# Kernel tuning notes

Measured on AMD Instinct MI355X. Metric: run time of the kernel, lower is better.

The kernel has to match this reference:

```python
import jax, jax.numpy as jnp
import numpy as np

B, OBS, T, H = 4096, 16, 32, 512  # batch, encoder length, decode seq_len, hidden_size


def _lstm_cell(x, h, c, Wi, Wh, b):
    # PyTorch gate order: i, f, g, o. b = b_ih + b_hh (mathematically identical).
    g = x @ Wi.T + h @ Wh.T + b
    i, f, gg, o = jnp.split(g, 4, axis=-1)
    c = jax.nn.sigmoid(f) * c + jax.nn.sigmoid(i) * jnp.tanh(gg)
    h = jax.nn.sigmoid(o) * jnp.tanh(c)
    return h, c


def _encode(xs, Wi, Wh, b):
    # xs: [B, T, 4]; returns final (h, c), zero initial state as in nn.LSTM.
    def step(carry, x):
        h, c = _lstm_cell(x, carry[0], carry[1], Wi, Wh, b)
        return (h, c), None
    z = jnp.zeros((xs.shape[0], H), xs.dtype)
    (h, c), _ = jax.lax.scan(step, (z, z), jnp.swapaxes(xs, 0, 1))
    return h, c


def setup_inputs() -> dict:
    key = jax.random.key(0)
    ks = jax.random.split(key, 22)
    s = 0.05
    p = lambda k, shape: (jax.random.normal(k, shape, jnp.float32) * s)
    return {
        "speed": jax.random.normal(ks[0], (B, OBS, 4), jnp.float32),
        "pos": jax.random.normal(ks[1], (B, OBS, 4), jnp.float32),
        "enc_s_Wi": p(ks[2], (4 * H, 4)), "enc_s_Wh": p(ks[3], (4 * H, H)), "enc_s_b": p(ks[4], (4 * H,)),
        "enc_p_Wi": p(ks[5], (4 * H, 4)), "enc_p_Wh": p(ks[6], (4 * H, H)), "enc_p_b": p(ks[7], (4 * H,)),
        "dec_s_Wi": p(ks[8], (4 * H, 4)), "dec_s_Wh": p(ks[9], (4 * H, H)), "dec_s_b": p(ks[10], (4 * H,)),
        "dec_i_Wi": p(ks[11], (4 * H, 4)), "dec_i_Wh": p(ks[12], (4 * H, H)), "dec_i_b": p(ks[13], (4 * H,)),
        "W_fs": p(ks[14], (4, H)), "b_fs": p(ks[15], (4,)),
        "W_fc": p(ks[16], (2, H)), "b_fc": p(ks[17], (2,)),
        "W_emb": p(ks[18], (4, 2)), "b_emb": p(ks[19], (4,)),
    }


def reference(speed, pos,
              enc_s_Wi, enc_s_Wh, enc_s_b,
              enc_p_Wi, enc_p_Wh, enc_p_b,
              dec_s_Wi, dec_s_Wh, dec_s_b,
              dec_i_Wi, dec_i_Wh, dec_i_b,
              W_fs, b_fs, W_fc, b_fc, W_emb, b_emb):
    h_se, c_se = _encode(speed, enc_s_Wi, enc_s_Wh, enc_s_b)
    h_pe, c_pe = _encode(pos, enc_p_Wi, enc_p_Wh, enc_p_b)
    h_s, c_s = h_se + h_pe, c_se + c_pe
    h_i, c_i = h_s, c_s
    last_speed = speed[:, -1, :]
    last_pos = pos[:, -1, :]

    def step(carry, _):
        h_s, c_s, h_i, c_i, ls, lp = carry
        h_s, c_s = _lstm_cell(ls, h_s, c_s, dec_s_Wi, dec_s_Wh, dec_s_b)
        h_i, c_i = _lstm_cell(lp, h_i, c_i, dec_i_Wi, dec_i_Wh, dec_i_b)
        sp = jnp.clip(h_s @ W_fs.T + b_fs, -100.0, 100.0)        # Hardtanh(-100, 100)
        it = jax.nn.relu(h_i @ W_fc.T + b_fc)                     # fc_crossing
        ls = jax.lax.stop_gradient(sp)                            # .detach()
        lp = jax.lax.stop_gradient(jax.nn.relu(it @ W_emb.T + b_emb))  # pos_embedding(.).detach()
        return (h_s, c_s, h_i, c_i, ls, lp), (sp, jax.nn.softmax(it, axis=1))

    carry0 = (h_s, c_s, h_i, c_i, last_speed, last_pos)
    _, (speed_seq, cross_seq) = jax.lax.scan(step, carry0, None, length=T)
    speed_outputs = jnp.swapaxes(speed_seq, 0, 1)   # [B, T, 4]
    # Faithful to the source bug: intention_outputs is never accumulated, so the
    # returned crossing_outputs holds ONLY the last step's softmax: [B, 1, 2].
    crossing_outputs = cross_seq[-1][:, None, :]
    return speed_outputs, crossing_outputs
```

## Files before the change

### kernel.cpp

```cpp
#include <hip/hip_runtime.h>
#include <stdint.h>

#define H 512
#define KAUG 528
#define KT_N 33
#define LROW 536
#define NROW 32
#define WMAT_ELEMS (16 * KT_N * 4 * 512)
#define T_DEC 32
#define B_TOT 4096

typedef __attribute__((ext_vector_type(8))) short short8;
typedef __attribute__((ext_vector_type(16))) float floatx16;

__device__ __forceinline__ unsigned short f2bf(float x) {
  union { float f; unsigned int u; } v; v.f = x;
  unsigned int u = v.u;
  return (unsigned short)((u + 0x7FFFu + ((u >> 16) & 1u)) >> 16);
}
__device__ __forceinline__ float bf2f(unsigned short s) {
  union { unsigned int u; float f; } v; v.u = ((unsigned int)s) << 16;
  return v.f;
}
__device__ __forceinline__ float rcpf(float x) { return __builtin_amdgcn_rcpf(x); }
__device__ __forceinline__ float sigm(float x) { return rcpf(1.0f + __expf(-x)); }
__device__ __forceinline__ float tanh_f(float x) {
  return 1.0f - 2.0f * rcpf(1.0f + __expf(2.0f * x));
}

#define MFMA(A, B, C) __builtin_amdgcn_mfma_f32_32x32x16_bf16(A, B, C, 0, 0, 0)

__global__ void prep_weights(
    const float* __restrict__ Wh_s, const float* __restrict__ Wi_s, const float* __restrict__ b_s,
    const float* __restrict__ Wh_p, const float* __restrict__ Wi_p, const float* __restrict__ b_p,
    const float* __restrict__ Wh_d, const float* __restrict__ Wi_d, const float* __restrict__ b_d,
    const float* __restrict__ Wh_i, const float* __restrict__ Wi_i, const float* __restrict__ b_i,
    short* __restrict__ wpack)
{
  int idx = blockIdx.x * 256 + threadIdx.x;
  const int per = 2048 * KAUG;
  if (idx >= 4 * per) return;
  int mat = idx / per;
  int rem = idx - mat * per;
  int n = rem / KAUG;
  int ka = rem - n * KAUG;
  const float* Wh; const float* Wi; const float* bb;
  if (mat == 0)      { Wh = Wh_s; Wi = Wi_s; bb = b_s; }
  else if (mat == 1) { Wh = Wh_p; Wi = Wi_p; bb = b_p; }
  else if (mat == 2) { Wh = Wh_d; Wi = Wi_d; bb = b_d; }
  else               { Wh = Wh_i; Wi = Wi_i; bb = b_i; }
  float v;
  if (ka < 512)      v = Wh[n * 512 + ka];
  else if (ka < 516) v = Wi[n * 4 + (ka - 512)];
  else if (ka == 516) v = bb[n];
  else               v = 0.0f;
  int g = n >> 9, ntL = (n >> 5) & 15, ni = n & 31;
  int kt = ka >> 4, kh = (ka >> 3) & 1, ks = ka & 7;
  int lanep = kh * 32 + ni;
  wpack[(size_t)mat * WMAT_ELEMS +
        (((((size_t)ntL * KT_N + kt) * 4 + g) << 9) + (lanep << 3) + ks)] = (short)f2bf(v);
}

__device__ __forceinline__ void lstm_step_mfma(
    const short* hl, const short* __restrict__ wm,
    int lane, int wv, float c_reg[16], float hnew[16])
{
  int arow = lane & 31, ahalf = lane >> 5;
  const short* aptr = hl + arow * LROW + ahalf * 8;
  const short* bp = wm + (size_t)wv * (KT_N * 4 * 512) + (lane << 3);
  floatx16 ai = (floatx16)0.0f, af = (floatx16)0.0f, ag = (floatx16)0.0f, ao = (floatx16)0.0f;
  short8 b00 = *(const short8*)(bp +    0), b01 = *(const short8*)(bp +  512);
  short8 b02 = *(const short8*)(bp + 1024), b03 = *(const short8*)(bp + 1536);
  short8 b10 = *(const short8*)(bp + 2048), b11 = *(const short8*)(bp + 2560);
  short8 b12 = *(const short8*)(bp + 3072), b13 = *(const short8*)(bp + 3584);
  #pragma unroll 2
  for (int kt = 0; kt < 32; kt += 2) {
    short8 a0 = *(const short8*)(aptr + kt * 16);
    ai = MFMA(a0, b00, ai); af = MFMA(a0, b01, af);
    ag = MFMA(a0, b02, ag); ao = MFMA(a0, b03, ao);
    {
      const short* np = bp + (kt + 2) * 2048;
      b00 = *(const short8*)(np);        b01 = *(const short8*)(np + 512);
      b02 = *(const short8*)(np + 1024); b03 = *(const short8*)(np + 1536);
    }
    short8 a1 = *(const short8*)(aptr + kt * 16 + 16);
    ai = MFMA(a1, b10, ai); af = MFMA(a1, b11, af);
    ag = MFMA(a1, b12, ag); ao = MFMA(a1, b13, ao);
    if (kt < 30) {
      const short* np = bp + (kt + 3) * 2048;
      b10 = *(const short8*)(np);        b11 = *(const short8*)(np + 512);
      b12 = *(const short8*)(np + 1024); b13 = *(const short8*)(np + 1536);
    }
  }
  {
    short8 a0 = *(const short8*)(aptr + 512);
    ai = MFMA(a0, b00, ai); af = MFMA(a0, b01, af);
    ag = MFMA(a0, b02, ag); ao = MFMA(a0, b03, ao);
  }
  #pragma unroll
  for (int r = 0; r < 16; ++r) {
    float si = sigm(ai[r]);
    float sf = sigm(af[r]);
    float tg = tanh_f(ag[r]);
    float so = sigm(ao[r]);
    float cn = sf * c_reg[r] + si * tg;
    c_reg[r] = cn;
    hnew[r] = so * tanh_f(cn);
  }
}

__device__ __forceinline__ void write_h(short* hl, int lane, int wv, const float hnew[16]) {
  int arow = lane & 31, ahalf = lane >> 5;
  int col = (wv << 5) + arow;
  #pragma unroll
  for (int r = 0; r < 16; ++r) {
    int row = (r & 3) + ((r >> 2) << 3) + (ahalf << 2);
    hl[row * LROW + col] = (short)f2bf(hnew[r]);
  }
}

__global__ __launch_bounds__(1024) void lstm_encoder(
    const float* __restrict__ speed, const float* __restrict__ pos,
    const short* __restrict__ wpack,
    short* __restrict__ h_enc, float* __restrict__ c_enc)
{
  __shared__ short hl[2][NROW * LROW];
  int tid = threadIdx.x;
  int b = blockIdx.x;
  int xcd = b & 7, slot = b >> 3;
  int enc = xcd >> 2;
  int rg = slot * 4 + (xcd & 3);
  int r0 = rg * 32;
  const float* xin = enc ? pos : speed;
  const short* wm = wpack + (size_t)enc * WMAT_ELEMS;

  {
    short* hz = &hl[0][0];
    for (int i = tid; i < 2 * NROW * LROW; i += 1024) hz[i] = 0;
  }
  __syncthreads();
  if (tid < 64) hl[tid >> 5][(tid & 31) * LROW + 516] = (short)0x3F80;
  if (tid < 128) {
    int r = tid >> 2, c = tid & 3;
    hl[0][r * LROW + 512 + c] = (short)f2bf(xin[(r0 + r) * 64 + c]);
  }
  __syncthreads();

  int lane = tid & 63, wv = tid >> 6;
  float c_reg[16];
  #pragma unroll
  for (int r = 0; r < 16; ++r) c_reg[r] = 0.0f;
  float hnew[16];

  for (int t = 0; t < 16; ++t) {
    const short* cb = hl[t & 1];
    short* nb = &hl[(t + 1) & 1][0];
    lstm_step_mfma(cb, wm, lane, wv, c_reg, hnew);
    write_h(nb, lane, wv, hnew);
    if (t < 15 && tid < 128) {
      int r = tid >> 2, c = tid & 3;
      nb[r * LROW + 512 + c] = (short)f2bf(xin[(r0 + r) * 64 + (t + 1) * 4 + c]);
    }
    __syncthreads();
  }

  for (int i = tid; i < 32 * 512; i += 1024) {
    int r = i >> 9, k = i & 511;
    h_enc[((size_t)(enc * B_TOT + r0 + r) << 9) + k] = hl[0][r * LROW + k];
  }
  int arow = lane & 31, ahalf = lane >> 5;
  int col = (wv << 5) + arow;
  #pragma unroll
  for (int r = 0; r < 16; ++r) {
    int row = (r & 3) + ((r >> 2) << 3) + (ahalf << 2);
    c_enc[((size_t)(enc * B_TOT + r0 + row) << 9) + col] = c_reg[r];
  }
}

__global__ __launch_bounds__(1024) void lstm_decoder(
    const float* __restrict__ speed, const float* __restrict__ pos,
    const short* __restrict__ wpack,
    const short* __restrict__ h_enc, const float* __restrict__ c_enc,
    const float* __restrict__ W_fs, const float* __restrict__ b_fs,
    const float* __restrict__ W_fc, const float* __restrict__ b_fc,
    const float* __restrict__ W_emb, const float* __restrict__ b_emb,
    float* __restrict__ out)
{
  __shared__ short hl[2][NROW * LROW];
  int tid = threadIdx.x;
  int b = blockIdx.x;
  int xcd = b & 7, slot = b >> 3;
  int chain = xcd >> 2;
  int rg = slot * 4 + (xcd & 3);
  int r0 = rg * 32;
  const short* wm = wpack + (size_t)(2 + chain) * WMAT_ELEMS;

  {
    short* hz = &hl[0][0];
    for (int i = tid; i < 2 * NROW * LROW; i += 1024) hz[i] = 0;
  }
  __syncthreads();
  for (int i = tid; i < 32 * 512; i += 1024) {
    int r = i >> 9, k = i & 511;
    float h0 = bf2f((unsigned short)h_enc[((size_t)(r0 + r) << 9) + k])
             + bf2f((unsigned short)h_enc[((size_t)(B_TOT + r0 + r) << 9) + k]);
    hl[0][r * LROW + k] = (short)f2bf(h0);
  }
  if (tid < 64) hl[tid >> 5][(tid & 31) * LROW + 516] = (short)0x3F80;
  {
    const float* last = chain ? pos : speed;
    if (tid < 128) {
      int r = tid >> 2, c = tid & 3;
      hl[0][r * LROW + 512 + c] = (short)f2bf(last[(r0 + r) * 64 + 60 + c]);
    }
  }
  int lane = tid & 63, wv = tid >> 6;
  int arow = lane & 31, ahalf = lane >> 5;
  float c_reg[16];
  {
    int col = (wv << 5) + arow;
    #pragma unroll
    for (int r = 0; r < 16; ++r) {
      int row = (r & 3) + ((r >> 2) << 3) + (ahalf << 2);
      size_t gi = ((size_t)(r0 + row) << 9) + col;
      c_reg[r] = c_enc[gi] + c_enc[gi + (((size_t)B_TOT) << 9)];
    }
  }
  __syncthreads();

  float hnew[16];
  for (int t = 0; t < T_DEC; ++t) {
    const short* cb = hl[t & 1];
    short* nb = &hl[(t + 1) & 1][0];
    lstm_step_mfma(cb, wm, lane, wv, c_reg, hnew);
    write_h(nb, lane, wv, hnew);
    __syncthreads();
    for (int r = 0; r < 2; ++r) {
      int row = wv * 2 + r;
      const short8 hvs = *(const short8*)(nb + row * LROW + lane * 8);
      float hv[8];
      #pragma unroll
      for (int j = 0; j < 8; ++j) hv[j] = bf2f((unsigned short)hvs[j]);
      if (chain == 0) {
        float p0 = 0.f, p1 = 0.f, p2 = 0.f, p3 = 0.f;
        #pragma unroll
        for (int j = 0; j < 8; ++j) {
          p0 += hv[j] * W_fs[0 * 512 + lane * 8 + j];
          p1 += hv[j] * W_fs[1 * 512 + lane * 8 + j];
          p2 += hv[j] * W_fs[2 * 512 + lane * 8 + j];
          p3 += hv[j] * W_fs[3 * 512 + lane * 8 + j];
        }
        #pragma unroll
        for (int off = 32; off > 0; off >>= 1) {
          p0 += __shfl_xor(p0, off);
          p1 += __shfl_xor(p1, off);
          p2 += __shfl_xor(p2, off);
          p3 += __shfl_xor(p3, off);
        }
        float s0 = fminf(fmaxf(p0 + b_fs[0], -100.0f), 100.0f);
        float s1 = fminf(fmaxf(p1 + b_fs[1], -100.0f), 100.0f);
        float s2 = fminf(fmaxf(p2 + b_fs[2], -100.0f), 100.0f);
        float s3 = fminf(fmaxf(p3 + b_fs[3], -100.0f), 100.0f);
        if (lane < 4) {
          float v = (lane == 0) ? s0 : (lane == 1) ? s1 : (lane == 2) ? s2 : s3;
          out[(size_t)(r0 + row) * 128 + t * 4 + lane] = v;
          nb[row * LROW + 512 + lane] = (short)f2bf(v);
        }
      } else {
        float p0 = 0.f, p1 = 0.f;
        #pragma unroll
        for (int j = 0; j < 8; ++j) {
          p0 += hv[j] * W_fc[0 * 512 + lane * 8 + j];
          p1 += hv[j] * W_fc[1 * 512 + lane * 8 + j];
        }
        #pragma unroll
        for (int off = 32; off > 0; off >>= 1) {
          p0 += __shfl_xor(p0, off);
          p1 += __shfl_xor(p1, off);
        }
        float it0 = fmaxf(p0 + b_fc[0], 0.0f);
        float it1 = fmaxf(p1 + b_fc[1], 0.0f);
        if (lane < 4) {
          float lp = fmaxf(W_emb[lane * 2] * it0 + W_emb[lane * 2 + 1] * it1 + b_emb[lane], 0.0f);
          nb[row * LROW + 512 + lane] = (short)f2bf(lp);
        }
        if (t == T_DEC - 1 && lane < 2) {
          float m = fmaxf(it0, it1);
          float e0 = __expf(it0 - m), e1 = __expf(it1 - m);
          float v = ((lane == 0) ? e0 : e1) * rcpf(e0 + e1);
          out[(size_t)524288 + (size_t)(r0 + row) * 2 + lane] = v;
        }
      }
    }
    __syncthreads();
  }
}

extern "C" void kernel_launch(void* const* d_in, const int* in_sizes, int n_in,
                              void* d_out, int out_size, void* d_ws, size_t ws_size,
                              hipStream_t stream)
{
  const float* speed    = (const float*)d_in[0];
  const float* pos      = (const float*)d_in[1];
  const float* enc_s_Wi = (const float*)d_in[2];
  const float* enc_s_Wh = (const float*)d_in[3];
  const float* enc_s_b  = (const float*)d_in[4];
  const float* enc_p_Wi = (const float*)d_in[5];
  const float* enc_p_Wh = (const float*)d_in[6];
  const float* enc_p_b  = (const float*)d_in[7];
  const float* dec_s_Wi = (const float*)d_in[8];
  const float* dec_s_Wh = (const float*)d_in[9];
  const float* dec_s_b  = (const float*)d_in[10];
  const float* dec_i_Wi = (const float*)d_in[11];
  const float* dec_i_Wh = (const float*)d_in[12];
  const float* dec_i_b  = (const float*)d_in[13];
  const float* W_fs     = (const float*)d_in[14];
  const float* b_fs     = (const float*)d_in[15];
  const float* W_fc     = (const float*)d_in[16];
  const float* b_fc     = (const float*)d_in[17];
  const float* W_emb    = (const float*)d_in[18];
  const float* b_emb    = (const float*)d_in[19];
  float* out = (float*)d_out;

  char* ws = (char*)d_ws;
  short* wpack = (short*)ws;
  short* h_enc = (short*)(ws + 8650752);
  float* c_enc = (float*)(ws + 17039360);

  prep_weights<<<16896, 256, 0, stream>>>(
      enc_s_Wh, enc_s_Wi, enc_s_b,
      enc_p_Wh, enc_p_Wi, enc_p_b,
      dec_s_Wh, dec_s_Wi, dec_s_b,
      dec_i_Wh, dec_i_Wi, dec_i_b,
      wpack);
  lstm_encoder<<<256, 1024, 0, stream>>>(speed, pos, wpack, h_enc, c_enc);
  lstm_decoder<<<256, 1024, 0, stream>>>(speed, pos, wpack, h_enc, c_enc,
                                         W_fs, b_fs, W_fc, b_fc, W_emb, b_emb, out);
}
```

Measured before the change: 1.452 ms.

## Split decoder step barrier so the output head overlaps the next recurrent matmul

The decoder's LSTM step is inlined and split. The 32 hidden-state k-tiles of the gate matmul now run before a barrier, and only the final k-tile (fed input, bias and ones) runs after it. The barrier at the end of each step is removed, so one step's output-head work (projections, shuffles, writing the next input columns) can overlap the next step's main matmul. The hand-written double-buffered B-operand prefetch is replaced, in both encoder and decoder, by a simple per-k-tile load-then-MFMA loop with unroll pragmas. That leaves load latency hiding to the compiler and may expose global-load stalls.

```diff
diff --git a/kernel.cpp b/kernel.cpp
--- a/kernel.cpp
+++ b/kernel.cpp
@@ -69,33 +69,16 @@
   const short* aptr = hl + arow * LROW + ahalf * 8;
   const short* bp = wm + (size_t)wv * (KT_N * 4 * 512) + (lane << 3);
   floatx16 ai = (floatx16)0.0f, af = (floatx16)0.0f, ag = (floatx16)0.0f, ao = (floatx16)0.0f;
-  short8 b00 = *(const short8*)(bp +    0), b01 = *(const short8*)(bp +  512);
-  short8 b02 = *(const short8*)(bp + 1024), b03 = *(const short8*)(bp + 1536);
-  short8 b10 = *(const short8*)(bp + 2048), b11 = *(const short8*)(bp + 2560);
-  short8 b12 = *(const short8*)(bp + 3072), b13 = *(const short8*)(bp + 3584);
-  #pragma unroll 2
-  for (int kt = 0; kt < 32; kt += 2) {
-    short8 a0 = *(const short8*)(aptr + kt * 16);
-    ai = MFMA(a0, b00, ai); af = MFMA(a0, b01, af);
-    ag = MFMA(a0, b02, ag); ao = MFMA(a0, b03, ao);
-    {
-      const short* np = bp + (kt + 2) * 2048;
-      b00 = *(const short8*)(np);        b01 = *(const short8*)(np + 512);
-      b02 = *(const short8*)(np + 1024); b03 = *(const short8*)(np + 1536);
-    }
-    short8 a1 = *(const short8*)(aptr + kt * 16 + 16);
-    ai = MFMA(a1, b10, ai); af = MFMA(a1, b11, af);
-    ag = MFMA(a1, b12, ag); ao = MFMA(a1, b13, ao);
-    if (kt < 30) {
-      const short* np = bp + (kt + 3) * 2048;
-      b10 = *(const short8*)(np);        b11 = *(const short8*)(np + 512);
-      b12 = *(const short8*)(np + 1024); b13 = *(const short8*)(np + 1536);
-    }
-  }
-  {
-    short8 a0 = *(const short8*)(aptr + 512);
-    ai = MFMA(a0, b00, ai); af = MFMA(a0, b01, af);
-    ag = MFMA(a0, b02, ag); ao = MFMA(a0, b03, ao);
+  #pragma unroll 3
+  for (int kt = 0; kt < KT_N; ++kt) {
+    short8 a  = *(const short8*)(aptr + kt * 16);
+    short8 b0 = *(const short8*)(bp);
+    short8 b1 = *(const short8*)(bp + 512);
+    short8 b2 = *(const short8*)(bp + 1024);
+    short8 b3 = *(const short8*)(bp + 1536);
+    bp += 2048;
+    ai = MFMA(a, b0, ai); af = MFMA(a, b1, af);
+    ag = MFMA(a, b2, ag); ao = MFMA(a, b3, ao);
   }
   #pragma unroll
   for (int r = 0; r < 16; ++r) {
@@ -109,7 +92,7 @@
   }
 }
 
-__device__ __forceinline__ void write_h(short* hl, int lane, int wv, const float hnew[16]) {
+__device__ __forceinline__ void write_h16(short* hl, int lane, int wv, const float hnew[16]) {
   int arow = lane & 31, ahalf = lane >> 5;
   int col = (wv << 5) + arow;
   #pragma unroll
@@ -156,7 +139,7 @@
     const short* cb = hl[t & 1];
     short* nb = &hl[(t + 1) & 1][0];
     lstm_step_mfma(cb, wm, lane, wv, c_reg, hnew);
-    write_h(nb, lane, wv, hnew);
+    write_h16(nb, lane, wv, hnew);
     if (t < 15 && tid < 128) {
       int r = tid >> 2, c = tid & 3;
       nb[r * LROW + 512 + c] = (short)f2bf(xin[(r0 + r) * 64 + (t + 1) * 4 + c]);
@@ -194,6 +177,8 @@
   int rg = slot * 4 + (xcd & 3);
   int r0 = rg * 32;
   const short* wm = wpack + (size_t)(2 + chain) * WMAT_ELEMS;
+  int lane = tid & 63, wv = tid >> 6;
+  int arow = lane & 31, ahalf = lane >> 5;
 
   {
     short* hz = &hl[0][0];
@@ -214,8 +199,7 @@
       hl[0][r * LROW + 512 + c] = (short)f2bf(last[(r0 + r) * 64 + 60 + c]);
     }
   }
-  int lane = tid & 63, wv = tid >> 6;
-  int arow = lane & 31, ahalf = lane >> 5;
+
   float c_reg[16];
   {
     int col = (wv << 5) + arow;
@@ -232,9 +216,47 @@
   for (int t = 0; t < T_DEC; ++t) {
     const short* cb = hl[t & 1];
     short* nb = &hl[(t + 1) & 1][0];
-    lstm_step_mfma(cb, wm, lane, wv, c_reg, hnew);
-    write_h(nb, lane, wv, hnew);
+    const short* aptr = cb + arow * LROW + ahalf * 8;
+    const short* bp = wm + (size_t)wv * (KT_N * 4 * 512) + (lane << 3);
+
+    floatx16 ai = (floatx16)0.0f, af = (floatx16)0.0f,
+             ag = (floatx16)0.0f, ao = (floatx16)0.0f;
+    #pragma unroll 4
+    for (int kt = 0; kt < 32; ++kt) {
+      short8 a  = *(const short8*)(aptr + kt * 16);
+      short8 b0 = *(const short8*)(bp);
+      short8 b1 = *(const short8*)(bp + 512);
+      short8 b2 = *(const short8*)(bp + 1024);
+      short8 b3 = *(const short8*)(bp + 1536);
+      bp += 2048;
+      ai = MFMA(a, b0, ai); af = MFMA(a, b1, af);
+      ag = MFMA(a, b2, ag); ao = MFMA(a, b3, ao);
+    }
     __syncthreads();
+    {
+      short8 a  = *(const short8*)(aptr + 512);
+      short8 b0 = *(const short8*)(bp);
+      short8 b1 = *(const short8*)(bp + 512);
+      short8 b2 = *(const short8*)(bp + 1024);
+      short8 b3 = *(const short8*)(bp + 1536);
+      ai = MFMA(a, b0, ai); af = MFMA(a, b1, af);
+      ag = MFMA(a, b2, ag); ao = MFMA(a, b3, ao);
+    }
+
+    #pragma unroll
+    for (int r = 0; r < 16; ++r) {
+      float si = sigm(ai[r]);
+      float sf = sigm(af[r]);
+      float tg = tanh_f(ag[r]);
+      float so = sigm(ao[r]);
+      float cn = sf * c_reg[r] + si * tg;
+      c_reg[r] = cn;
+      hnew[r] = so * tanh_f(cn);
+    }
+    write_h16(nb, lane, wv, hnew);
+    __syncthreads();
+
+    #pragma unroll 1
     for (int r = 0; r < 2; ++r) {
       int row = wv * 2 + r;
       const short8 hvs = *(const short8*)(nb + row * LROW + lane * 8);
@@ -292,7 +314,6 @@
         }
       }
     }
-    __syncthreads();
   }
 }
 
```

Result: faster. 1.291 ms (-11.1%).
